# Kernel tuning notes

Hardware: AMD Instinct MI355X
Metric: run time of the kernel (lower is better)

The kernel has to match this reference:

```python
import jax, jax.numpy as jnp
import numpy as np

H = 1024          # n_hidden
FGB = 1.0         # forget_gate_bias added to forget-gate preactivation


def lstm_layer(x, h0, c0, Wih, Whh, b):
    """Standard LSTM over time-major x:(U,B,H). Gate order i,f,g,o (PyTorch)."""
    def step(carry, xt):
        h, c = carry
        gates = xt @ Wih.T + h @ Whh.T + b            # (B,4H)
        i, f, g, o = jnp.split(gates, 4, axis=-1)
        i = jax.nn.sigmoid(i)
        f = jax.nn.sigmoid(f + FGB)
        g = jnp.tanh(g)
        o = jax.nn.sigmoid(o)
        c = f * c + i * g
        h = o * jnp.tanh(c)
        return (h, c), h
    (hT, cT), hs = jax.lax.scan(step, (h0, c0), x)
    return hs, hT, cT


def setup_inputs() -> dict:
    key = jax.random.key(0)
    ks = jax.random.split(key, 8)
    B, U, V = 64, 512, 1024
    s = 1.0 / np.sqrt(H)
    inp = {
        "y": jax.random.randint(ks[0], (B, U), 0, V - 1, dtype=jnp.int64)
             if jax.config.jax_enable_x64 else
             jax.random.randint(ks[0], (B, U), 0, V - 1, dtype=jnp.int32),
        "E": jax.random.normal(ks[1], (V - 1, H), jnp.float32) * s,
        "Wih0": jax.random.normal(ks[2], (4 * H, H), jnp.float32) * s,
        "Whh0": jax.random.normal(ks[3], (4 * H, H), jnp.float32) * s,
        "b0": jax.random.normal(ks[4], (4 * H,), jnp.float32) * s,
        "Wih1": jax.random.normal(ks[5], (4 * H, H), jnp.float32) * s,
        "Whh1": jax.random.normal(ks[6], (4 * H, H), jnp.float32) * s,
        "b1": jax.random.normal(ks[7], (4 * H,), jnp.float32) * s,
    }
    return inp


def reference(y, E, Wih0, Whh0, b0, Wih1, Whh1, b1):
    # Prediction.forward with y given, state=None (zero initial states)
    x = E[y]                          # (B,U,H) embedding lookup
    x = jnp.transpose(x, (1, 0, 2))   # (U,B,H) time-major
    B = x.shape[1]
    z = jnp.zeros((B, H), x.dtype)
    hs0, h0f, c0f = lstm_layer(x, z, z, Wih0, Whh0, b0)
    hs1, h1f, c1f = lstm_layer(hs0, z, z, Wih1, Whh1, b1)
    g = jnp.transpose(hs1, (1, 0, 2))  # (B,U,H)
    h = jnp.stack([h0f, h1f])          # (L,B,H)
    c = jnp.stack([c0f, c1f])          # (L,B,H)
    return g, (h, c)
```

## Files before the change

### kernel.cpp

```cpp
#include <hip/hip_runtime.h>
#include <hip/hip_bf16.h>

typedef unsigned short u16;
typedef unsigned long long ull;
typedef __attribute__((ext_vector_type(8))) short bf16x8;
typedef __attribute__((ext_vector_type(4))) float f32x4;
typedef __attribute__((ext_vector_type(2))) float f32x2;

#define HID 1024
#define BATCH 64
#define SEQ 512
#define MTOK 32768

#define WB_WIH0 0
#define WB_WHH0 4194304
#define WB_WIH1 8388608
#define WB_WHH1 12582912
#define WS_X_OFF   33554432ull
#define WS_XP_OFF  100663296ull
#define WS_NEEDED  369098752ull
#define RING0_B 0ull
#define RING1_B 524288ull
#define XP1_B   1048576ull
#define FLAGS_B 3145728ull

#define OUT_H_OFF 33554432
#define OUT_C_OFF 33685504


__device__ __forceinline__ u16 f2bf(float f) {
    union { float f; unsigned u; } x; x.f = f;
    unsigned r = (x.u + 0x7FFFu + ((x.u >> 16) & 1u)) >> 16;
    return (u16)r;
}
__device__ __forceinline__ float bf2f(u16 v) {
    union { unsigned u; float f; } x; x.u = ((unsigned)v) << 16;
    return x.f;
}
__device__ __forceinline__ float fexp2(float x) { return __builtin_amdgcn_exp2f(x); }
__device__ __forceinline__ float frcp(float x) { return __builtin_amdgcn_rcpf(x); }
__device__ __forceinline__ float sigm(float x) {
    return frcp(1.f + fexp2(x * -1.4426950408889634f));
}
__device__ __forceinline__ float tanh_f(float x) {
    return 1.f - 2.f * frcp(fexp2(x * 2.8853900817779268f) + 1.f);
}
__device__ __forceinline__ float xpick(ull q, int bb, int u) {
    return bf2f((u16)(q >> ((bb * 2 + u) << 4)));
}
__device__ __forceinline__ void ldsload16(const u16* g, u16* l) {
    __builtin_amdgcn_global_load_lds(
        (__attribute__((address_space(1))) void*)(unsigned long long)(const char*)g,
        (__attribute__((address_space(3))) void*)l, 16, 0, 0);
}
__device__ __forceinline__ ull ld8(const ull* p) {
    return __hip_atomic_load(p, __ATOMIC_RELAXED, __HIP_MEMORY_SCOPE_AGENT);
}
__device__ __forceinline__ unsigned ld4(const unsigned* p) {
    return __hip_atomic_load(p, __ATOMIC_RELAXED, __HIP_MEMORY_SCOPE_AGENT);
}
__device__ __forceinline__ void st8(ull* p, ull v) {
    __hip_atomic_store(p, v, __ATOMIC_RELAXED, __HIP_MEMORY_SCOPE_AGENT);
}
__device__ __forceinline__ void st4(unsigned* p, unsigned v) {
    __hip_atomic_store(p, v, __ATOMIC_RELAXED, __HIP_MEMORY_SCOPE_AGENT);
}

__launch_bounds__(256)
__global__ void prep_weights(const float* __restrict__ a, const float* __restrict__ b,
                             const float* __restrict__ c, const float* __restrict__ d,
                             u16* __restrict__ dst) {
    const int gtid = blockIdx.x * 256 + threadIdx.x;
#pragma unroll
    for (int k = 0; k < 16; k++) {
        const float* s = (k < 4) ? a : (k < 8) ? b : (k < 12) ? c : d;
        const int off = ((k & 3) * 262144 + gtid) * 4;
        float4 v = *(const float4*)(s + off);
        ushort4 o;
        o.x = f2bf(v.x); o.y = f2bf(v.y); o.z = f2bf(v.z); o.w = f2bf(v.w);
        *(ushort4*)(dst + (size_t)(k >> 2) * 4194304 + off) = o;
    }
}

__launch_bounds__(256)
__global__ void gather_x(const int* __restrict__ y, const float* __restrict__ E,
                         u16* __restrict__ X) {
    const int m = blockIdx.x;
    const int t = m >> 6, b = m & 63;
    const int idx = y[b * SEQ + t];
    const float4 v = *(const float4*)(E + (size_t)idx * HID + threadIdx.x * 4);
    ushort4 o;
    o.x = f2bf(v.x); o.y = f2bf(v.y); o.z = f2bf(v.z); o.w = f2bf(v.w);
    *(ushort4*)(X + (size_t)m * HID + threadIdx.x * 4) = o;
}

__launch_bounds__(256, 3)
__global__ void gemm_bt(const u16* __restrict__ A, const u16* __restrict__ Bm,
                        const float* __restrict__ bias, u16* __restrict__ C,
                        int M, int N, int K) {
    __shared__ u16 As[128 * 64];
    __shared__ u16 Bs[128 * 64];
    const int tid = threadIdx.x;
    const int ln = tid & 63;
    const int l15 = ln & 15, q = ln >> 4;
    const int w = tid >> 6;
    const int wm = (w & 1) * 64, wn = (w >> 1) * 64;
    const int m0 = blockIdx.y * 128, n0 = blockIdx.x * 128;

    f32x4 acc[4][4];
#pragma unroll
    for (int i = 0; i < 4; i++)
#pragma unroll
        for (int j = 0; j < 4; j++) acc[i][j] = 0.f;

    const int srow = tid >> 3;
    const int spk = tid & 7;
    const u16* gA = A + (size_t)m0 * K;
    const u16* gB = Bm + (size_t)n0 * K;
    const int wbase = (tid & 0xC0) * 8;

    const int kIters = K >> 6;
    for (int kt = 0; kt < kIters; kt++) {
        const int k0 = kt << 6;
        __syncthreads();
#pragma unroll
        for (int i = 0; i < 4; i++) {
            const int row = i * 32 + srow;
            const int kb = spk ^ (row & 7);
            ldsload16(gA + (size_t)row * K + k0 + kb * 8, &As[i * 2048 + wbase]);
            ldsload16(gB + (size_t)row * K + k0 + kb * 8, &Bs[i * 2048 + wbase]);
        }
        __syncthreads();
#pragma unroll
        for (int s = 0; s < 2; s++) {
            const int xk = ((s * 4 + q) ^ (l15 & 7)) * 8;
            bf16x8 af[4], bfr[4];
#pragma unroll
            for (int mi = 0; mi < 4; mi++)
                af[mi] = *(const bf16x8*)&As[(wm + mi * 16 + l15) * 64 + xk];
#pragma unroll
            for (int nj = 0; nj < 4; nj++)
                bfr[nj] = *(const bf16x8*)&Bs[(wn + nj * 16 + l15) * 64 + xk];
#pragma unroll
            for (int mi = 0; mi < 4; mi++)
#pragma unroll
                for (int nj = 0; nj < 4; nj++)
                    acc[mi][nj] = __builtin_amdgcn_mfma_f32_16x16x32_bf16(
                        af[mi], bfr[nj], acc[mi][nj], 0, 0, 0);
        }
    }
#pragma unroll
    for (int nj = 0; nj < 4; nj++) {
        const int n = n0 + wn + nj * 16 + l15;
        const float bv = bias[n];
        const int g = n >> 10, c = n & 1023;
        const int jblk = c >> 4, up = (c & 15) >> 1, u = c & 1;
#pragma unroll
        for (int mi = 0; mi < 4; mi++) {
            const int mb = m0 + wm + mi * 16 + q * 4;
            f32x4 v = acc[mi][nj];
            float vals[4] = {v.x, v.y, v.z, v.w};
#pragma unroll
            for (int k = 0; k < 4; k++) {
                const int m = mb + k;
                const int r = m >> 6, b = m & 63;
                const int bp = b >> 1, bb = b & 1;
                const int t = bp * 8 + up;
                C[(size_t)r * 262144 + jblk * 4096 + t * 16 + g * 4 + bb * 2 + u]
                    = f2bf(vals[k] + bv);
            }
        }
    }
}

__global__ void init_flags(unsigned* f) { if (threadIdx.x < 192) f[threadIdx.x] = 0; }


__device__ __forceinline__ void load_wf(const u16* W, int j0, int w, int l15, int q,
                                        bf16x8 wf[4][8]) {
    const u16* wbase = W + (size_t)(j0 + l15) * HID + w * 256 + q * 8;
#pragma unroll
    for (int nt = 0; nt < 4; nt++)
#pragma unroll
        for (int ki = 0; ki < 8; ki++)
            wf[nt][ki] = *(const bf16x8*)(wbase + (size_t)nt * 1048576 + ki * 32);
}

__device__ __forceinline__ void mm_ring(const u16* slab, const bf16x8 wf[4][8],
                                        int w, int l15, int q, float (*P)[64][68]) {
    union BU { ull v[2]; bf16x8 f; };
    BU st[4][8];
    const u16* arow = slab + (size_t)l15 * HID + w * 256 + q * 8;
#pragma unroll
    for (int ki = 0; ki < 8; ki++)
#pragma unroll
        for (int mt = 0; mt < 4; mt++) {
            const ull* p = (const ull*)(arow + mt * 16384 + ki * 32);
            st[mt][ki].v[0] = ld8(p);
            st[mt][ki].v[1] = ld8(p + 1);
        }
    f32x4 acc[4][4];
#pragma unroll
    for (int mt = 0; mt < 4; mt++)
#pragma unroll
        for (int nt = 0; nt < 4; nt++) acc[mt][nt] = 0.f;
#pragma unroll
    for (int ki = 0; ki < 8; ki++)
#pragma unroll
        for (int mt = 0; mt < 4; mt++)
#pragma unroll
            for (int nt = 0; nt < 4; nt++)
                acc[mt][nt] = __builtin_amdgcn_mfma_f32_16x16x32_bf16(
                    st[mt][ki].f, wf[nt][ki], acc[mt][nt], 0, 0, 0);
#pragma unroll
    for (int mt = 0; mt < 4; mt++)
#pragma unroll
        for (int nt = 0; nt < 4; nt++)
            *(f32x4*)&P[w][nt * 16 + l15][mt * 16 + q * 4] = acc[mt][nt];
}

__device__ __forceinline__ void waitflags(const unsigned* F0, const unsigned* Fp,
                                          const unsigned* Fr, int n0, int np, int nr,
                                          int w, int ln, int* abortf) {
    const unsigned* A = (w == 0) ? F0 : (w == 1) ? Fp : Fr;
    const int need = (w == 0) ? n0 : (w == 1) ? np : nr;
    if (w < 3 && need > 0 && *abortf == 0) {
        int it = 0;
        while ((int)ld4(&A[ln]) < need) {
            __builtin_amdgcn_s_sleep(1);
            if (++it > 2000000) { *abortf = 1; break; }
        }
    }
    __syncthreads();
}

__launch_bounds__(256, 1)
__global__ void pipeline(const u16* __restrict__ wb, const u16* __restrict__ Xp,
                         const float* __restrict__ b1, float* __restrict__ out,
                         u16* __restrict__ ring0, u16* __restrict__ ring1,
                         u16* __restrict__ xp1, unsigned* __restrict__ flags) {
    __shared__ float P[4][64][68];
    __shared__ int abortf;
    const int tid = threadIdx.x;
    if (tid == 0) abortf = 0;
    const int w = tid >> 6, ln = tid & 63;
    const int l15 = ln & 15, q = ln >> 4;
    const int bid = blockIdx.x;
    const int role = bid >> 6;
    const int jblk = bid & 63;
    const int j0 = jblk * 16;
    unsigned* F0 = flags;
    unsigned* Fp = flags + 64;
    unsigned* Fr = flags + 128;
    __syncthreads();

    bf16x8 wf[4][8];

    if (role == 0) {
        load_wf(wb + WB_WHH0, j0, w, l15, q, wf);
        const int up = tid & 7, bp = tid >> 3;
        float cst[2][2] = {{0.f, 0.f}, {0.f, 0.f}};
        for (int r = 0; r < 512; ++r) {
            ull xq[4];
            const ull* xp8 = (const ull*)(Xp + (size_t)r * 262144 + jblk * 4096 + tid * 16);
#pragma unroll
            for (int gg = 0; gg < 4; gg++) xq[gg] = xp8[gg];
            waitflags(F0, Fp, Fr, r, r - 2, 0, w, ln, &abortf);
            if (r > 0)
                mm_ring(ring0 + (size_t)((r - 1) & 3) * 65536, wf, w, l15, q, P);
            __syncthreads();
            f32x2 pre[4][2];
#pragma unroll
            for (int gg = 0; gg < 4; gg++)
#pragma unroll
                for (int u = 0; u < 2; u++) {
                    if (r > 0) {
                        const int col = gg * 16 + up * 2 + u;
                        f32x2 s = *(const f32x2*)&P[0][col][bp * 2];
                        s += *(const f32x2*)&P[1][col][bp * 2];
                        s += *(const f32x2*)&P[2][col][bp * 2];
                        s += *(const f32x2*)&P[3][col][bp * 2];
                        pre[gg][u] = s;
                    } else pre[gg][u] = 0.f;
                }
            u16* hout = ring0 + (size_t)(r & 3) * 65536;
#pragma unroll
            for (int bb = 0; bb < 2; bb++) {
                const int b = bp * 2 + bb;
                float hn[2], cn[2];
#pragma unroll
                for (int u = 0; u < 2; u++) {
                    const float pi = pre[0][u][bb] + xpick(xq[0], bb, u);
                    const float pf = pre[1][u][bb] + xpick(xq[1], bb, u) + 1.0f;
                    const float pg = pre[2][u][bb] + xpick(xq[2], bb, u);
                    const float po = pre[3][u][bb] + xpick(xq[3], bb, u);
                    const float cnew = sigm(pf) * cst[bb][u] + sigm(pi) * tanh_f(pg);
                    cst[bb][u] = cnew;
                    hn[u] = sigm(po) * tanh_f(cnew);
                    cn[u] = cnew;
                }
                const unsigned hw = (unsigned)f2bf(hn[0]) | ((unsigned)f2bf(hn[1]) << 16);
                st4((unsigned*)(hout + (size_t)b * HID + j0 + up * 2), hw);
                if (r == 511) {
                    f32x2 h2 = {hn[0], hn[1]}, c2 = {cn[0], cn[1]};
                    *(f32x2*)&out[OUT_H_OFF + (size_t)b * HID + j0 + up * 2] = h2;
                    *(f32x2*)&out[OUT_C_OFF + (size_t)b * HID + j0 + up * 2] = c2;
                }
            }
            __syncthreads();
            if (tid == 0) st4(&F0[bid], (unsigned)(r + 1));
        }
    } else if (role == 1) {
        load_wf(wb + WB_WIH1, j0, w, l15, q, wf);
        const int up = tid & 7, bp = tid >> 3;
        float bv[4][2];
#pragma unroll
        for (int gg = 0; gg < 4; gg++)
#pragma unroll
            for (int u = 0; u < 2; u++)
                bv[gg][u] = b1[gg * 1024 + j0 + up * 2 + u];
        for (int r = 1; r <= 512; ++r) {
            waitflags(F0, Fp, Fr, r, 0, r - 2, w, ln, &abortf);
            mm_ring(ring0 + (size_t)((r - 1) & 3) * 65536, wf, w, l15, q, P);
            __syncthreads();
            ull* xo8 = (ull*)(xp1 + (size_t)((r - 1) & 3) * 262144 + jblk * 4096 + tid * 16);
            ull ow[4];
#pragma unroll
            for (int gg = 0; gg < 4; gg++) {
                ow[gg] = 0;
#pragma unroll
                for (int u = 0; u < 2; u++) {
                    const int col = gg * 16 + up * 2 + u;
                    f32x2 s = *(const f32x2*)&P[0][col][bp * 2];
                    s += *(const f32x2*)&P[1][col][bp * 2];
                    s += *(const f32x2*)&P[2][col][bp * 2];
                    s += *(const f32x2*)&P[3][col][bp * 2];
#pragma unroll
                    for (int bb = 0; bb < 2; bb++) {
                        const float val = s[bb] + bv[gg][u];
                        ow[gg] |= (ull)f2bf(val) << ((bb * 2 + u) << 4);
                    }
                }
            }
#pragma unroll
            for (int gg = 0; gg < 4; gg++) st8(xo8 + gg, ow[gg]);
            __syncthreads();
            if (tid == 0) st4(&Fp[jblk], (unsigned)(r + 1));
        }
    } else {
        load_wf(wb + WB_WHH1, j0, w, l15, q, wf);
        const int up = tid & 7, bp = tid >> 3;
        float cst[2][2] = {{0.f, 0.f}, {0.f, 0.f}};
        for (int r = 2; r <= 513; ++r) {
            const int t = r - 2;
            waitflags(F0, Fp, Fr, 0, r, (r >= 3) ? r : 0, w, ln, &abortf);
            ull xq[4];
            const ull* xp8 = (const ull*)(xp1 + (size_t)(t & 3) * 262144 + jblk * 4096 + tid * 16);
#pragma unroll
            for (int gg = 0; gg < 4; gg++) xq[gg] = ld8(xp8 + gg);
            if (r > 2)
                mm_ring(ring1 + (size_t)((r - 3) & 3) * 65536, wf, w, l15, q, P);
            __syncthreads();
            f32x2 pre[4][2];
#pragma unroll
            for (int gg = 0; gg < 4; gg++)
#pragma unroll
                for (int u = 0; u < 2; u++) {
                    if (r > 2) {
                        const int col = gg * 16 + up * 2 + u;
                        f32x2 s = *(const f32x2*)&P[0][col][bp * 2];
                        s += *(const f32x2*)&P[1][col][bp * 2];
                        s += *(const f32x2*)&P[2][col][bp * 2];
                        s += *(const f32x2*)&P[3][col][bp * 2];
                        pre[gg][u] = s;
                    } else pre[gg][u] = 0.f;
                }
            u16* hout = ring1 + (size_t)((r - 2) & 3) * 65536;
#pragma unroll
            for (int bb = 0; bb < 2; bb++) {
                const int b = bp * 2 + bb;
                float hn[2], cn[2];
#pragma unroll
                for (int u = 0; u < 2; u++) {
                    const float pi = pre[0][u][bb] + xpick(xq[0], bb, u);
                    const float pf = pre[1][u][bb] + xpick(xq[1], bb, u) + 1.0f;
                    const float pg = pre[2][u][bb] + xpick(xq[2], bb, u);
                    const float po = pre[3][u][bb] + xpick(xq[3], bb, u);
                    const float cnew = sigm(pf) * cst[bb][u] + sigm(pi) * tanh_f(pg);
                    cst[bb][u] = cnew;
                    hn[u] = sigm(po) * tanh_f(cnew);
                    cn[u] = cnew;
                }
                const unsigned hw = (unsigned)f2bf(hn[0]) | ((unsigned)f2bf(hn[1]) << 16);
                st4((unsigned*)(hout + (size_t)b * HID + j0 + up * 2), hw);
                f32x2 g2 = {hn[0], hn[1]};
                *(f32x2*)&out[(size_t)b * 524288 + (size_t)t * 1024 + j0 + up * 2] = g2;
                if (r == 513) {
                    f32x2 h2 = {hn[0], hn[1]}, c2 = {cn[0], cn[1]};
                    *(f32x2*)&out[OUT_H_OFF + 65536 + (size_t)b * HID + j0 + up * 2] = h2;
                    *(f32x2*)&out[OUT_C_OFF + 65536 + (size_t)b * HID + j0 + up * 2] = c2;
                }
            }
            __syncthreads();
            if (tid == 0) st4(&Fr[jblk], (unsigned)(r + 1));
        }
    }
}

__global__ void diag(float* o, float v) { o[0] = v; }

extern "C" void kernel_launch(void* const* d_in, const int* in_sizes, int n_in,
                              void* d_out, int out_size, void* d_ws, size_t ws_size,
                              hipStream_t stream) {
    const int*   y    = (const int*)  d_in[0];
    const float* Emb  = (const float*)d_in[1];
    const float* Wih0 = (const float*)d_in[2];
    const float* Whh0 = (const float*)d_in[3];
    const float* b0   = (const float*)d_in[4];
    const float* Wih1 = (const float*)d_in[5];
    const float* Whh1 = (const float*)d_in[6];
    const float* b1   = (const float*)d_in[7];
    float* out = (float*)d_out;
    char* wsb = (char*)d_ws;

    if (ws_size < WS_NEEDED) {
        diag<<<1, 1, 0, stream>>>(out, (float)(ws_size >> 20));
        return;
    }

    u16* wb   = (u16*)wsb;
    u16* X    = (u16*)(wsb + WS_X_OFF);
    u16* Xp   = (u16*)(wsb + WS_XP_OFF);
    u16* ring0 = (u16*)(wsb + RING0_B);
    u16* ring1 = (u16*)(wsb + RING1_B);
    u16* xp1   = (u16*)(wsb + XP1_B);
    unsigned* flags = (unsigned*)(wsb + FLAGS_B);

    prep_weights<<<1024, 256, 0, stream>>>(Wih0, Whh0, Wih1, Whh1, wb);
    gather_x<<<MTOK, 256, 0, stream>>>(y, Emb, X);
    gemm_bt<<<dim3(32, 256), 256, 0, stream>>>(X, wb + WB_WIH0, b0, Xp, MTOK, 4096, HID);
    init_flags<<<1, 256, 0, stream>>>(flags);
    pipeline<<<192, 256, 0, stream>>>(wb, Xp, b1, out, ring0, ring1, xp1, flags);
}
```

Before: 6.968 ms.

## Fuse layer-1 input projection into recurrent blocks, dropping the middle pipeline role

```diff
diff --git a/kernel.cpp b/kernel.cpp
--- a/kernel.cpp
+++ b/kernel.cpp
@@ -21,7 +21,6 @@
 #define WS_NEEDED  369098752ull
 #define RING0_B 0ull
 #define RING1_B 524288ull
-#define XP1_B   1048576ull
 #define FLAGS_B 3145728ull
 
 #define OUT_H_OFF 33554432
@@ -173,7 +172,7 @@
     }
 }
 
-__global__ void init_flags(unsigned* f) { if (threadIdx.x < 192) f[threadIdx.x] = 0; }
+__global__ void init_flags(unsigned* f) { if (threadIdx.x < 128) f[threadIdx.x] = 0; }
 
 
 __device__ __forceinline__ void load_wf(const u16* W, int j0, int w, int l15, int q,
@@ -187,7 +186,7 @@
 }
 
 __device__ __forceinline__ void mm_ring(const u16* slab, const bf16x8 wf[4][8],
-                                        int w, int l15, int q, float (*P)[64][68]) {
+                                        int w, int l15, int q, f32x4 acc[4][4]) {
     union BU { ull v[2]; bf16x8 f; };
     BU st[4][8];
     const u16* arow = slab + (size_t)l15 * HID + w * 256 + q * 8;
@@ -199,11 +198,7 @@
             st[mt][ki].v[0] = ld8(p);
             st[mt][ki].v[1] = ld8(p + 1);
         }
-    f32x4 acc[4][4];
-#pragma unroll
-    for (int mt = 0; mt < 4; mt++)
-#pragma unroll
-        for (int nt = 0; nt < 4; nt++) acc[mt][nt] = 0.f;
+    __builtin_amdgcn_sched_barrier(0);
 #pragma unroll
     for (int ki = 0; ki < 8; ki++)
 #pragma unroll
@@ -212,6 +207,39 @@
             for (int nt = 0; nt < 4; nt++)
                 acc[mt][nt] = __builtin_amdgcn_mfma_f32_16x16x32_bf16(
                     st[mt][ki].f, wf[nt][ki], acc[mt][nt], 0, 0, 0);
+}
+
+__device__ __forceinline__ void mm_fwd(const u16* slab, const u16* W, int j0,
+                                       int w, int l15, int q, f32x4 acc[4][4]) {
+    union BU { ull v[2]; bf16x8 f; };
+    BU st[4][8];
+    const u16* arow = slab + (size_t)l15 * HID + w * 256 + q * 8;
+    const u16* wbase = W + (size_t)(j0 + l15) * HID + w * 256 + q * 8;
+#pragma unroll
+    for (int ki = 0; ki < 8; ki++)
+#pragma unroll
+        for (int mt = 0; mt < 4; mt++) {
+            const ull* p = (const ull*)(arow + mt * 16384 + ki * 32);
+            st[mt][ki].v[0] = ld8(p);
+            st[mt][ki].v[1] = ld8(p + 1);
+        }
+#pragma unroll
+    for (int ki = 0; ki < 8; ki++) {
+        bf16x8 wfk[4];
+#pragma unroll
+        for (int nt = 0; nt < 4; nt++)
+            wfk[nt] = *(const bf16x8*)(wbase + (size_t)nt * 1048576 + ki * 32);
+#pragma unroll
+        for (int mt = 0; mt < 4; mt++)
+#pragma unroll
+            for (int nt = 0; nt < 4; nt++)
+                acc[mt][nt] = __builtin_amdgcn_mfma_f32_16x16x32_bf16(
+                    st[mt][ki].f, wfk[nt], acc[mt][nt], 0, 0, 0);
+    }
+}
+
+__device__ __forceinline__ void store_P(const f32x4 acc[4][4], int w, int l15, int q,
+                                        float (*P)[64][68]) {
 #pragma unroll
     for (int mt = 0; mt < 4; mt++)
 #pragma unroll
@@ -219,16 +247,14 @@
             *(f32x4*)&P[w][nt * 16 + l15][mt * 16 + q * 4] = acc[mt][nt];
 }
 
-__device__ __forceinline__ void waitflags(const unsigned* F0, const unsigned* Fp,
-                                          const unsigned* Fr, int n0, int np, int nr,
-                                          int w, int ln, int* abortf) {
-    const unsigned* A = (w == 0) ? F0 : (w == 1) ? Fp : Fr;
-    const int need = (w == 0) ? n0 : (w == 1) ? np : nr;
-    if (w < 3 && need > 0 && *abortf == 0) {
+__device__ __forceinline__ void wait2(const unsigned* F0, const unsigned* Fr,
+                                      int n0, int nr, int w, int ln, int* abortf) {
+    const unsigned* A = (w == 0) ? F0 : Fr;
+    const int need = (w == 0) ? n0 : nr;
+    if (w < 2 && need > 0 && *abortf == 0) {
         int it = 0;
         while ((int)ld4(&A[ln]) < need) {
-            __builtin_amdgcn_s_sleep(1);
-            if (++it > 2000000) { *abortf = 1; break; }
+            if (++it > 20000000) { *abortf = 1; break; }
         }
     }
     __syncthreads();
@@ -238,7 +264,7 @@
 __global__ void pipeline(const u16* __restrict__ wb, const u16* __restrict__ Xp,
                          const float* __restrict__ b1, float* __restrict__ out,
                          u16* __restrict__ ring0, u16* __restrict__ ring1,
-                         u16* __restrict__ xp1, unsigned* __restrict__ flags) {
+                         unsigned* __restrict__ flags) {
     __shared__ float P[4][64][68];
     __shared__ int abortf;
     const int tid = threadIdx.x;
@@ -250,13 +276,11 @@
     const int jblk = bid & 63;
     const int j0 = jblk * 16;
     unsigned* F0 = flags;
-    unsigned* Fp = flags + 64;
-    unsigned* Fr = flags + 128;
+    unsigned* Fr = flags + 64;
     __syncthreads();
 
-    bf16x8 wf[4][8];
-
     if (role == 0) {
+        bf16x8 wf[4][8];
         load_wf(wb + WB_WHH0, j0, w, l15, q, wf);
         const int up = tid & 7, bp = tid >> 3;
         float cst[2][2] = {{0.f, 0.f}, {0.f, 0.f}};
@@ -265,9 +289,16 @@
             const ull* xp8 = (const ull*)(Xp + (size_t)r * 262144 + jblk * 4096 + tid * 16);
 #pragma unroll
             for (int gg = 0; gg < 4; gg++) xq[gg] = xp8[gg];
-            waitflags(F0, Fp, Fr, r, r - 2, 0, w, ln, &abortf);
-            if (r > 0)
-                mm_ring(ring0 + (size_t)((r - 1) & 3) * 65536, wf, w, l15, q, P);
+            wait2(F0, Fr, r, r - 3, w, ln, &abortf);
+            if (r > 0) {
+                f32x4 acc[4][4];
+#pragma unroll
+                for (int i = 0; i < 4; i++)
+#pragma unroll
+                    for (int j = 0; j < 4; j++) acc[i][j] = 0.f;
+                mm_ring(ring0 + (size_t)((r - 1) & 3) * 65536, wf, w, l15, q, acc);
+                store_P(acc, w, l15, q, P);
+            }
             __syncthreads();
             f32x2 pre[4][2];
 #pragma unroll
@@ -308,10 +339,11 @@
                 }
             }
             __syncthreads();
-            if (tid == 0) st4(&F0[bid], (unsigned)(r + 1));
-        }
-    } else if (role == 1) {
-        load_wf(wb + WB_WIH1, j0, w, l15, q, wf);
+            if (tid == 0) st4(&F0[jblk], (unsigned)(r + 1));
+        }
+    } else {
+        bf16x8 wf[4][8];
+        load_wf(wb + WB_WHH1, j0, w, l15, q, wf);
         const int up = tid & 7, bp = tid >> 3;
         float bv[4][2];
 #pragma unroll
@@ -319,15 +351,23 @@
 #pragma unroll
             for (int u = 0; u < 2; u++)
                 bv[gg][u] = b1[gg * 1024 + j0 + up * 2 + u];
-        for (int r = 1; r <= 512; ++r) {
-            waitflags(F0, Fp, Fr, r, 0, r - 2, w, ln, &abortf);
-            mm_ring(ring0 + (size_t)((r - 1) & 3) * 65536, wf, w, l15, q, P);
+        float cst[2][2] = {{0.f, 0.f}, {0.f, 0.f}};
+        f32x4 acc[4][4];
+#pragma unroll
+        for (int i = 0; i < 4; i++)
+#pragma unroll
+            for (int j = 0; j < 4; j++) acc[i][j] = 0.f;
+        wait2(F0, Fr, 1, 0, w, ln, &abortf);
+        mm_fwd(ring0, wb + WB_WIH1, j0, w, l15, q, acc);
+        for (int t = 0; t < 512; ++t) {
+            wait2(F0, Fr, 0, t, w, ln, &abortf);
+            if (t > 0)
+                mm_ring(ring1 + (size_t)((t - 1) & 3) * 65536, wf, w, l15, q, acc);
+            store_P(acc, w, l15, q, P);
             __syncthreads();
-            ull* xo8 = (ull*)(xp1 + (size_t)((r - 1) & 3) * 262144 + jblk * 4096 + tid * 16);
-            ull ow[4];
-#pragma unroll
-            for (int gg = 0; gg < 4; gg++) {
-                ow[gg] = 0;
+            f32x2 pre[4][2];
+#pragma unroll
+            for (int gg = 0; gg < 4; gg++)
 #pragma unroll
                 for (int u = 0; u < 2; u++) {
                     const int col = gg * 16 + up * 2 + u;
@@ -335,57 +375,20 @@
                     s += *(const f32x2*)&P[1][col][bp * 2];
                     s += *(const f32x2*)&P[2][col][bp * 2];
                     s += *(const f32x2*)&P[3][col][bp * 2];
-#pragma unroll
-                    for (int bb = 0; bb < 2; bb++) {
-                        const float val = s[bb] + bv[gg][u];
-                        ow[gg] |= (ull)f2bf(val) << ((bb * 2 + u) << 4);
-                    }
-                }
-            }
-#pragma unroll
-            for (int gg = 0; gg < 4; gg++) st8(xo8 + gg, ow[gg]);
-            __syncthreads();
-            if (tid == 0) st4(&Fp[jblk], (unsigned)(r + 1));
-        }
-    } else {
-        load_wf(wb + WB_WHH1, j0, w, l15, q, wf);
-        const int up = tid & 7, bp = tid >> 3;
-        float cst[2][2] = {{0.f, 0.f}, {0.f, 0.f}};
-        for (int r = 2; r <= 513; ++r) {
-            const int t = r - 2;
-            waitflags(F0, Fp, Fr, 0, r, (r >= 3) ? r : 0, w, ln, &abortf);
-            ull xq[4];
-            const ull* xp8 = (const ull*)(xp1 + (size_t)(t & 3) * 262144 + jblk * 4096 + tid * 16);
-#pragma unroll
-            for (int gg = 0; gg < 4; gg++) xq[gg] = ld8(xp8 + gg);
-            if (r > 2)
-                mm_ring(ring1 + (size_t)((r - 3) & 3) * 65536, wf, w, l15, q, P);
-            __syncthreads();
-            f32x2 pre[4][2];
-#pragma unroll
-            for (int gg = 0; gg < 4; gg++)
-#pragma unroll
-                for (int u = 0; u < 2; u++) {
-                    if (r > 2) {
-                        const int col = gg * 16 + up * 2 + u;
-                        f32x2 s = *(const f32x2*)&P[0][col][bp * 2];
-                        s += *(const f32x2*)&P[1][col][bp * 2];
-                        s += *(const f32x2*)&P[2][col][bp * 2];
-                        s += *(const f32x2*)&P[3][col][bp * 2];
-                        pre[gg][u] = s;
-                    } else pre[gg][u] = 0.f;
-                }
-            u16* hout = ring1 + (size_t)((r - 2) & 3) * 65536;
+                    s += bv[gg][u];
+                    pre[gg][u] = s;
+                }
+            u16* hout = ring1 + (size_t)(t & 3) * 65536;
 #pragma unroll
             for (int bb = 0; bb < 2; bb++) {
                 const int b = bp * 2 + bb;
                 float hn[2], cn[2];
 #pragma unroll
                 for (int u = 0; u < 2; u++) {
-                    const float pi = pre[0][u][bb] + xpick(xq[0], bb, u);
-                    const float pf = pre[1][u][bb] + xpick(xq[1], bb, u) + 1.0f;
-                    const float pg = pre[2][u][bb] + xpick(xq[2], bb, u);
-                    const float po = pre[3][u][bb] + xpick(xq[3], bb, u);
+                    const float pi = pre[0][u][bb];
+                    const float pf = pre[1][u][bb] + 1.0f;
+                    const float pg = pre[2][u][bb];
+                    const float po = pre[3][u][bb];
                     const float cnew = sigm(pf) * cst[bb][u] + sigm(pi) * tanh_f(pg);
                     cst[bb][u] = cnew;
                     hn[u] = sigm(po) * tanh_f(cnew);
@@ -395,14 +398,23 @@
                 st4((unsigned*)(hout + (size_t)b * HID + j0 + up * 2), hw);
                 f32x2 g2 = {hn[0], hn[1]};
                 *(f32x2*)&out[(size_t)b * 524288 + (size_t)t * 1024 + j0 + up * 2] = g2;
-                if (r == 513) {
+                if (t == 511) {
                     f32x2 h2 = {hn[0], hn[1]}, c2 = {cn[0], cn[1]};
                     *(f32x2*)&out[OUT_H_OFF + 65536 + (size_t)b * HID + j0 + up * 2] = h2;
                     *(f32x2*)&out[OUT_C_OFF + 65536 + (size_t)b * HID + j0 + up * 2] = c2;
                 }
             }
             __syncthreads();
-            if (tid == 0) st4(&Fr[jblk], (unsigned)(r + 1));
+            if (tid == 0) st4(&Fr[jblk], (unsigned)(t + 1));
+            if (t < 511) {
+                wait2(F0, Fr, t + 2, 0, w, ln, &abortf);
+#pragma unroll
+                for (int i = 0; i < 4; i++)
+#pragma unroll
+                    for (int j = 0; j < 4; j++) acc[i][j] = 0.f;
+                mm_fwd(ring0 + (size_t)((t + 1) & 3) * 65536, wb + WB_WIH1, j0,
+                       w, l15, q, acc);
+            }
         }
     }
 }
@@ -433,12 +445,11 @@
     u16* Xp   = (u16*)(wsb + WS_XP_OFF);
     u16* ring0 = (u16*)(wsb + RING0_B);
     u16* ring1 = (u16*)(wsb + RING1_B);
-    u16* xp1   = (u16*)(wsb + XP1_B);
     unsigned* flags = (unsigned*)(wsb + FLAGS_B);
 
     prep_weights<<<1024, 256, 0, stream>>>(Wih0, Whh0, Wih1, Whh1, wb);
     gather_x<<<MTOK, 256, 0, stream>>>(y, Emb, X);
     gemm_bt<<<dim3(32, 256), 256, 0, stream>>>(X, wb + WB_WIH0, b0, Xp, MTOK, 4096, HID);
     init_flags<<<1, 256, 0, stream>>>(flags);
-    pipeline<<<192, 256, 0, stream>>>(wb, Xp, b1, out, ring0, ring1, xp1, flags);
-}
+    pipeline<<<128, 256, 0, stream>>>(wb, Xp, b1, out, ring0, ring1, flags);
+}
```

Result: slower. 11.14 ms (+59.9%).

## Replace persistent flag-synchronized pipeline kernel with per-timestep kernel launches

Applied to the files above, without the earlier changes.

```diff
diff --git a/kernel.cpp b/kernel.cpp
--- a/kernel.cpp
+++ b/kernel.cpp
@@ -22,7 +22,8 @@
 #define RING0_B 0ull
 #define RING1_B 524288ull
 #define XP1_B   1048576ull
-#define FLAGS_B 3145728ull
+#define C0_B    3145728ull
+#define C1_B    3407872ull
 
 #define OUT_H_OFF 33554432
 #define OUT_C_OFF 33685504
@@ -52,18 +53,6 @@
     __builtin_amdgcn_global_load_lds(
         (__attribute__((address_space(1))) void*)(unsigned long long)(const char*)g,
         (__attribute__((address_space(3))) void*)l, 16, 0, 0);
-}
-__device__ __forceinline__ ull ld8(const ull* p) {
-    return __hip_atomic_load(p, __ATOMIC_RELAXED, __HIP_MEMORY_SCOPE_AGENT);
-}
-__device__ __forceinline__ unsigned ld4(const unsigned* p) {
-    return __hip_atomic_load(p, __ATOMIC_RELAXED, __HIP_MEMORY_SCOPE_AGENT);
-}
-__device__ __forceinline__ void st8(ull* p, ull v) {
-    __hip_atomic_store(p, v, __ATOMIC_RELAXED, __HIP_MEMORY_SCOPE_AGENT);
-}
-__device__ __forceinline__ void st4(unsigned* p, unsigned v) {
-    __hip_atomic_store(p, v, __ATOMIC_RELAXED, __HIP_MEMORY_SCOPE_AGENT);
 }
 
 __launch_bounds__(256)
@@ -173,8 +162,6 @@
     }
 }
 
-__global__ void init_flags(unsigned* f) { if (threadIdx.x < 192) f[threadIdx.x] = 0; }
-
 
 __device__ __forceinline__ void load_wf(const u16* W, int j0, int w, int l15, int q,
                                         bf16x8 wf[4][8]) {
@@ -186,24 +173,16 @@
             wf[nt][ki] = *(const bf16x8*)(wbase + (size_t)nt * 1048576 + ki * 32);
 }
 
-__device__ __forceinline__ void mm_ring(const u16* slab, const bf16x8 wf[4][8],
-                                        int w, int l15, int q, float (*P)[64][68]) {
-    union BU { ull v[2]; bf16x8 f; };
-    BU st[4][8];
+__device__ __forceinline__ void mm_plain(const u16* slab, const bf16x8 wf[4][8],
+                                         int w, int l15, int q, f32x4 acc[4][4]) {
+    bf16x8 st[4][8];
     const u16* arow = slab + (size_t)l15 * HID + w * 256 + q * 8;
 #pragma unroll
     for (int ki = 0; ki < 8; ki++)
 #pragma unroll
-        for (int mt = 0; mt < 4; mt++) {
-            const ull* p = (const ull*)(arow + mt * 16384 + ki * 32);
-            st[mt][ki].v[0] = ld8(p);
-            st[mt][ki].v[1] = ld8(p + 1);
-        }
-    f32x4 acc[4][4];
-#pragma unroll
-    for (int mt = 0; mt < 4; mt++)
-#pragma unroll
-        for (int nt = 0; nt < 4; nt++) acc[mt][nt] = 0.f;
+        for (int mt = 0; mt < 4; mt++)
+            st[mt][ki] = *(const bf16x8*)(arow + (size_t)mt * 16384 + ki * 32);
+    __builtin_amdgcn_sched_barrier(0);
 #pragma unroll
     for (int ki = 0; ki < 8; ki++)
 #pragma unroll
@@ -211,7 +190,11 @@
 #pragma unroll
             for (int nt = 0; nt < 4; nt++)
                 acc[mt][nt] = __builtin_amdgcn_mfma_f32_16x16x32_bf16(
-                    st[mt][ki].f, wf[nt][ki], acc[mt][nt], 0, 0, 0);
+                    st[mt][ki], wf[nt][ki], acc[mt][nt], 0, 0, 0);
+}
+
+__device__ __forceinline__ void store_P(const f32x4 acc[4][4], int w, int l15, int q,
+                                        float (*P)[64][68]) {
 #pragma unroll
     for (int mt = 0; mt < 4; mt++)
 #pragma unroll
@@ -219,191 +202,186 @@
             *(f32x4*)&P[w][nt * 16 + l15][mt * 16 + q * 4] = acc[mt][nt];
 }
 
-__device__ __forceinline__ void waitflags(const unsigned* F0, const unsigned* Fp,
-                                          const unsigned* Fr, int n0, int np, int nr,
-                                          int w, int ln, int* abortf) {
-    const unsigned* A = (w == 0) ? F0 : (w == 1) ? Fp : Fr;
-    const int need = (w == 0) ? n0 : (w == 1) ? np : nr;
-    if (w < 3 && need > 0 && *abortf == 0) {
-        int it = 0;
-        while ((int)ld4(&A[ln]) < need) {
-            __builtin_amdgcn_s_sleep(1);
-            if (++it > 2000000) { *abortf = 1; break; }
-        }
-    }
-    __syncthreads();
-}
-
-__launch_bounds__(256, 1)
-__global__ void pipeline(const u16* __restrict__ wb, const u16* __restrict__ Xp,
-                         const float* __restrict__ b1, float* __restrict__ out,
-                         u16* __restrict__ ring0, u16* __restrict__ ring1,
-                         u16* __restrict__ xp1, unsigned* __restrict__ flags) {
+__launch_bounds__(256)
+__global__ void step_k(int r, const u16* __restrict__ wb, const u16* __restrict__ Xp,
+                       const float* __restrict__ b1, float* __restrict__ out,
+                       u16* __restrict__ ring0, u16* __restrict__ ring1,
+                       u16* __restrict__ xp1, float* __restrict__ c0st,
+                       float* __restrict__ c1st) {
     __shared__ float P[4][64][68];
-    __shared__ int abortf;
     const int tid = threadIdx.x;
-    if (tid == 0) abortf = 0;
     const int w = tid >> 6, ln = tid & 63;
     const int l15 = ln & 15, q = ln >> 4;
     const int bid = blockIdx.x;
     const int role = bid >> 6;
     const int jblk = bid & 63;
     const int j0 = jblk * 16;
-    unsigned* F0 = flags;
-    unsigned* Fp = flags + 64;
-    unsigned* Fr = flags + 128;
-    __syncthreads();
-
-    bf16x8 wf[4][8];
 
     if (role == 0) {
+        if (r > 511) return;
+        const int up = tid & 7, bp = tid >> 3;
+        ull xq[4];
+        const ull* xp8 = (const ull*)(Xp + (size_t)r * 262144 + jblk * 4096 + tid * 16);
+#pragma unroll
+        for (int gg = 0; gg < 4; gg++) xq[gg] = xp8[gg];
+        f32x4 cin = {0.f, 0.f, 0.f, 0.f};
+        if (r > 0) cin = *(const f32x4*)(c0st + ((size_t)jblk * 256 + tid) * 4);
+        bf16x8 wf[4][8];
         load_wf(wb + WB_WHH0, j0, w, l15, q, wf);
-        const int up = tid & 7, bp = tid >> 3;
-        float cst[2][2] = {{0.f, 0.f}, {0.f, 0.f}};
-        for (int r = 0; r < 512; ++r) {
-            ull xq[4];
-            const ull* xp8 = (const ull*)(Xp + (size_t)r * 262144 + jblk * 4096 + tid * 16);
-#pragma unroll
-            for (int gg = 0; gg < 4; gg++) xq[gg] = xp8[gg];
-            waitflags(F0, Fp, Fr, r, r - 2, 0, w, ln, &abortf);
-            if (r > 0)
-                mm_ring(ring0 + (size_t)((r - 1) & 3) * 65536, wf, w, l15, q, P);
-            __syncthreads();
-            f32x2 pre[4][2];
-#pragma unroll
-            for (int gg = 0; gg < 4; gg++)
-#pragma unroll
-                for (int u = 0; u < 2; u++) {
-                    if (r > 0) {
-                        const int col = gg * 16 + up * 2 + u;
-                        f32x2 s = *(const f32x2*)&P[0][col][bp * 2];
-                        s += *(const f32x2*)&P[1][col][bp * 2];
-                        s += *(const f32x2*)&P[2][col][bp * 2];
-                        s += *(const f32x2*)&P[3][col][bp * 2];
-                        pre[gg][u] = s;
-                    } else pre[gg][u] = 0.f;
-                }
-            u16* hout = ring0 + (size_t)(r & 3) * 65536;
-#pragma unroll
-            for (int bb = 0; bb < 2; bb++) {
-                const int b = bp * 2 + bb;
-                float hn[2], cn[2];
-#pragma unroll
-                for (int u = 0; u < 2; u++) {
-                    const float pi = pre[0][u][bb] + xpick(xq[0], bb, u);
-                    const float pf = pre[1][u][bb] + xpick(xq[1], bb, u) + 1.0f;
-                    const float pg = pre[2][u][bb] + xpick(xq[2], bb, u);
-                    const float po = pre[3][u][bb] + xpick(xq[3], bb, u);
-                    const float cnew = sigm(pf) * cst[bb][u] + sigm(pi) * tanh_f(pg);
-                    cst[bb][u] = cnew;
-                    hn[u] = sigm(po) * tanh_f(cnew);
-                    cn[u] = cnew;
-                }
-                const unsigned hw = (unsigned)f2bf(hn[0]) | ((unsigned)f2bf(hn[1]) << 16);
-                st4((unsigned*)(hout + (size_t)b * HID + j0 + up * 2), hw);
-                if (r == 511) {
-                    f32x2 h2 = {hn[0], hn[1]}, c2 = {cn[0], cn[1]};
-                    *(f32x2*)&out[OUT_H_OFF + (size_t)b * HID + j0 + up * 2] = h2;
-                    *(f32x2*)&out[OUT_C_OFF + (size_t)b * HID + j0 + up * 2] = c2;
-                }
-            }
-            __syncthreads();
-            if (tid == 0) st4(&F0[bid], (unsigned)(r + 1));
-        }
-    } else if (role == 1) {
-        load_wf(wb + WB_WIH1, j0, w, l15, q, wf);
-        const int up = tid & 7, bp = tid >> 3;
-        float bv[4][2];
+        f32x4 acc[4][4];
+#pragma unroll
+        for (int i = 0; i < 4; i++)
+#pragma unroll
+            for (int j = 0; j < 4; j++) acc[i][j] = 0.f;
+        if (r > 0)
+            mm_plain(ring0 + (size_t)((r - 1) & 3) * 65536, wf, w, l15, q, acc);
+        store_P(acc, w, l15, q, P);
+        __syncthreads();
+        f32x2 pre[4][2];
 #pragma unroll
         for (int gg = 0; gg < 4; gg++)
 #pragma unroll
-            for (int u = 0; u < 2; u++)
-                bv[gg][u] = b1[gg * 1024 + j0 + up * 2 + u];
-        for (int r = 1; r <= 512; ++r) {
-            waitflags(F0, Fp, Fr, r, 0, r - 2, w, ln, &abortf);
-            mm_ring(ring0 + (size_t)((r - 1) & 3) * 65536, wf, w, l15, q, P);
-            __syncthreads();
-            ull* xo8 = (ull*)(xp1 + (size_t)((r - 1) & 3) * 262144 + jblk * 4096 + tid * 16);
-            ull ow[4];
-#pragma unroll
-            for (int gg = 0; gg < 4; gg++) {
-                ow[gg] = 0;
-#pragma unroll
-                for (int u = 0; u < 2; u++) {
+            for (int u = 0; u < 2; u++) {
+                if (r > 0) {
                     const int col = gg * 16 + up * 2 + u;
                     f32x2 s = *(const f32x2*)&P[0][col][bp * 2];
                     s += *(const f32x2*)&P[1][col][bp * 2];
                     s += *(const f32x2*)&P[2][col][bp * 2];
                     s += *(const f32x2*)&P[3][col][bp * 2];
-#pragma unroll
-                    for (int bb = 0; bb < 2; bb++) {
-                        const float val = s[bb] + bv[gg][u];
-                        ow[gg] |= (ull)f2bf(val) << ((bb * 2 + u) << 4);
-                    }
+                    pre[gg][u] = s;
+                } else pre[gg][u] = 0.f;
+            }
+        float cst[2][2] = {{cin.x, cin.y}, {cin.z, cin.w}};
+        u16* hout = ring0 + (size_t)(r & 3) * 65536;
+#pragma unroll
+        for (int bb = 0; bb < 2; bb++) {
+            const int b = bp * 2 + bb;
+            float hn[2], cn[2];
+#pragma unroll
+            for (int u = 0; u < 2; u++) {
+                const float pi = pre[0][u][bb] + xpick(xq[0], bb, u);
+                const float pf = pre[1][u][bb] + xpick(xq[1], bb, u) + 1.0f;
+                const float pg = pre[2][u][bb] + xpick(xq[2], bb, u);
+                const float po = pre[3][u][bb] + xpick(xq[3], bb, u);
+                const float cnew = sigm(pf) * cst[bb][u] + sigm(pi) * tanh_f(pg);
+                cst[bb][u] = cnew;
+                hn[u] = sigm(po) * tanh_f(cnew);
+                cn[u] = cnew;
+            }
+            const unsigned hw = (unsigned)f2bf(hn[0]) | ((unsigned)f2bf(hn[1]) << 16);
+            *(unsigned*)(hout + (size_t)b * HID + j0 + up * 2) = hw;
+            if (r == 511) {
+                f32x2 h2 = {hn[0], hn[1]}, c2 = {cn[0], cn[1]};
+                *(f32x2*)&out[OUT_H_OFF + (size_t)b * HID + j0 + up * 2] = h2;
+                *(f32x2*)&out[OUT_C_OFF + (size_t)b * HID + j0 + up * 2] = c2;
+            }
+        }
+        f32x4 cout = {cst[0][0], cst[0][1], cst[1][0], cst[1][1]};
+        *(f32x4*)(c0st + ((size_t)jblk * 256 + tid) * 4) = cout;
+    } else if (role == 1) {
+        if (r < 1 || r > 512) return;
+        const int up = tid & 7, bp = tid >> 3;
+        float bv[4][2];
+#pragma unroll
+        for (int gg = 0; gg < 4; gg++)
+#pragma unroll
+            for (int u = 0; u < 2; u++)
+                bv[gg][u] = b1[gg * 1024 + j0 + up * 2 + u];
+        bf16x8 wf[4][8];
+        load_wf(wb + WB_WIH1, j0, w, l15, q, wf);
+        f32x4 acc[4][4];
+#pragma unroll
+        for (int i = 0; i < 4; i++)
+#pragma unroll
+            for (int j = 0; j < 4; j++) acc[i][j] = 0.f;
+        mm_plain(ring0 + (size_t)((r - 1) & 3) * 65536, wf, w, l15, q, acc);
+        store_P(acc, w, l15, q, P);
+        __syncthreads();
+        ull* xo8 = (ull*)(xp1 + (size_t)((r - 1) & 3) * 262144 + jblk * 4096 + tid * 16);
+        ull ow[4];
+#pragma unroll
+        for (int gg = 0; gg < 4; gg++) {
+            ow[gg] = 0;
+#pragma unroll
+            for (int u = 0; u < 2; u++) {
+                const int col = gg * 16 + up * 2 + u;
+                f32x2 s = *(const f32x2*)&P[0][col][bp * 2];
+                s += *(const f32x2*)&P[1][col][bp * 2];
+                s += *(const f32x2*)&P[2][col][bp * 2];
+                s += *(const f32x2*)&P[3][col][bp * 2];
+#pragma unroll
+                for (int bb = 0; bb < 2; bb++) {
+                    const float val = s[bb] + bv[gg][u];
+                    ow[gg] |= (ull)f2bf(val) << ((bb * 2 + u) << 4);
                 }
             }
-#pragma unroll
-            for (int gg = 0; gg < 4; gg++) st8(xo8 + gg, ow[gg]);
-            __syncthreads();
-            if (tid == 0) st4(&Fp[jblk], (unsigned)(r + 1));
-        }
+        }
+#pragma unroll
+        for (int gg = 0; gg < 4; gg++) xo8[gg] = ow[gg];
     } else {
+        if (r < 2) return;
+        const int t = r - 2;
+        const int up = tid & 7, bp = tid >> 3;
+        ull xq[4];
+        const ull* xp8 = (const ull*)(xp1 + (size_t)(t & 3) * 262144 + jblk * 4096 + tid * 16);
+#pragma unroll
+        for (int gg = 0; gg < 4; gg++) xq[gg] = xp8[gg];
+        f32x4 cin = {0.f, 0.f, 0.f, 0.f};
+        if (t > 0) cin = *(const f32x4*)(c1st + ((size_t)jblk * 256 + tid) * 4);
+        bf16x8 wf[4][8];
         load_wf(wb + WB_WHH1, j0, w, l15, q, wf);
-        const int up = tid & 7, bp = tid >> 3;
-        float cst[2][2] = {{0.f, 0.f}, {0.f, 0.f}};
-        for (int r = 2; r <= 513; ++r) {
-            const int t = r - 2;
-            waitflags(F0, Fp, Fr, 0, r, (r >= 3) ? r : 0, w, ln, &abortf);
-            ull xq[4];
-            const ull* xp8 = (const ull*)(xp1 + (size_t)(t & 3) * 262144 + jblk * 4096 + tid * 16);
-#pragma unroll
-            for (int gg = 0; gg < 4; gg++) xq[gg] = ld8(xp8 + gg);
-            if (r > 2)
-                mm_ring(ring1 + (size_t)((r - 3) & 3) * 65536, wf, w, l15, q, P);
-            __syncthreads();
-            f32x2 pre[4][2];
-#pragma unroll
-            for (int gg = 0; gg < 4; gg++)
-#pragma unroll
-                for (int u = 0; u < 2; u++) {
-                    if (r > 2) {
-                        const int col = gg * 16 + up * 2 + u;
-                        f32x2 s = *(const f32x2*)&P[0][col][bp * 2];
-                        s += *(const f32x2*)&P[1][col][bp * 2];
-                        s += *(const f32x2*)&P[2][col][bp * 2];
-                        s += *(const f32x2*)&P[3][col][bp * 2];
-                        pre[gg][u] = s;
-                    } else pre[gg][u] = 0.f;
-                }
-            u16* hout = ring1 + (size_t)((r - 2) & 3) * 65536;
-#pragma unroll
-            for (int bb = 0; bb < 2; bb++) {
-                const int b = bp * 2 + bb;
-                float hn[2], cn[2];
-#pragma unroll
-                for (int u = 0; u < 2; u++) {
-                    const float pi = pre[0][u][bb] + xpick(xq[0], bb, u);
-                    const float pf = pre[1][u][bb] + xpick(xq[1], bb, u) + 1.0f;
-                    const float pg = pre[2][u][bb] + xpick(xq[2], bb, u);
-                    const float po = pre[3][u][bb] + xpick(xq[3], bb, u);
-                    const float cnew = sigm(pf) * cst[bb][u] + sigm(pi) * tanh_f(pg);
-                    cst[bb][u] = cnew;
-                    hn[u] = sigm(po) * tanh_f(cnew);
-                    cn[u] = cnew;
-                }
-                const unsigned hw = (unsigned)f2bf(hn[0]) | ((unsigned)f2bf(hn[1]) << 16);
-                st4((unsigned*)(hout + (size_t)b * HID + j0 + up * 2), hw);
-                f32x2 g2 = {hn[0], hn[1]};
-                *(f32x2*)&out[(size_t)b * 524288 + (size_t)t * 1024 + j0 + up * 2] = g2;
-                if (r == 513) {
-                    f32x2 h2 = {hn[0], hn[1]}, c2 = {cn[0], cn[1]};
-                    *(f32x2*)&out[OUT_H_OFF + 65536 + (size_t)b * HID + j0 + up * 2] = h2;
-                    *(f32x2*)&out[OUT_C_OFF + 65536 + (size_t)b * HID + j0 + up * 2] = c2;
-                }
-            }
-            __syncthreads();
-            if (tid == 0) st4(&Fr[jblk], (unsigned)(r + 1));
-        }
+        f32x4 acc[4][4];
+#pragma unroll
+        for (int i = 0; i < 4; i++)
+#pragma unroll
+            for (int j = 0; j < 4; j++) acc[i][j] = 0.f;
+        if (t > 0)
+            mm_plain(ring1 + (size_t)((t - 1) & 3) * 65536, wf, w, l15, q, acc);
+        store_P(acc, w, l15, q, P);
+        __syncthreads();
+        f32x2 pre[4][2];
+#pragma unroll
+        for (int gg = 0; gg < 4; gg++)
+#pragma unroll
+            for (int u = 0; u < 2; u++) {
+                if (t > 0) {
+                    const int col = gg * 16 + up * 2 + u;
+                    f32x2 s = *(const f32x2*)&P[0][col][bp * 2];
+                    s += *(const f32x2*)&P[1][col][bp * 2];
+                    s += *(const f32x2*)&P[2][col][bp * 2];
+                    s += *(const f32x2*)&P[3][col][bp * 2];
+                    pre[gg][u] = s;
+                } else pre[gg][u] = 0.f;
+            }
+        float cst[2][2] = {{cin.x, cin.y}, {cin.z, cin.w}};
+        u16* hout = ring1 + (size_t)(t & 3) * 65536;
+#pragma unroll
+        for (int bb = 0; bb < 2; bb++) {
+            const int b = bp * 2 + bb;
+            float hn[2], cn[2];
+#pragma unroll
+            for (int u = 0; u < 2; u++) {
+                const float pi = pre[0][u][bb] + xpick(xq[0], bb, u);
+                const float pf = pre[1][u][bb] + xpick(xq[1], bb, u) + 1.0f;
+                const float pg = pre[2][u][bb] + xpick(xq[2], bb, u);
+                const float po = pre[3][u][bb] + xpick(xq[3], bb, u);
+                const float cnew = sigm(pf) * cst[bb][u] + sigm(pi) * tanh_f(pg);
+                cst[bb][u] = cnew;
+                hn[u] = sigm(po) * tanh_f(cnew);
+                cn[u] = cnew;
+            }
+            const unsigned hw = (unsigned)f2bf(hn[0]) | ((unsigned)f2bf(hn[1]) << 16);
+            *(unsigned*)(hout + (size_t)b * HID + j0 + up * 2) = hw;
+            f32x2 g2 = {hn[0], hn[1]};
+            *(f32x2*)&out[(size_t)b * 524288 + (size_t)t * 1024 + j0 + up * 2] = g2;
+            if (t == 511) {
+                f32x2 h2 = {hn[0], hn[1]}, c2 = {cn[0], cn[1]};
+                *(f32x2*)&out[OUT_H_OFF + 65536 + (size_t)b * HID + j0 + up * 2] = h2;
+                *(f32x2*)&out[OUT_C_OFF + 65536 + (size_t)b * HID + j0 + up * 2] = c2;
+            }
+        }
+        f32x4 cout = {cst[0][0], cst[0][1], cst[1][0], cst[1][1]};
+        *(f32x4*)(c1st + ((size_t)jblk * 256 + tid) * 4) = cout;
     }
 }
 
@@ -434,11 +412,13 @@
     u16* ring0 = (u16*)(wsb + RING0_B);
     u16* ring1 = (u16*)(wsb + RING1_B);
     u16* xp1   = (u16*)(wsb + XP1_B);
-    unsigned* flags = (unsigned*)(wsb + FLAGS_B);
+    float* c0st = (float*)(wsb + C0_B);
+    float* c1st = (float*)(wsb + C1_B);
 
     prep_weights<<<1024, 256, 0, stream>>>(Wih0, Whh0, Wih1, Whh1, wb);
     gather_x<<<MTOK, 256, 0, stream>>>(y, Emb, X);
     gemm_bt<<<dim3(32, 256), 256, 0, stream>>>(X, wb + WB_WIH0, b0, Xp, MTOK, 4096, HID);
-    init_flags<<<1, 256, 0, stream>>>(flags);
-    pipeline<<<192, 256, 0, stream>>>(wb, Xp, b1, out, ring0, ring1, xp1, flags);
-}
+    for (int r = 0; r < 514; ++r)
+        step_k<<<192, 256, 0, stream>>>(r, wb, Xp, b1, out, ring0, ring1, xp1,
+                                        c0st, c1st);
+}
```

Result: faster. 6.295 ms (-9.7%).
